# Kernel tuning notes

Hardware: AMD Instinct MI355X
Metric: run time of the kernel (lower is better)

## Reference

```python
import math
import jax, jax.numpy as jnp
import numpy as np

DIM, HEADS, HD = 384, 12, 32
FEAT, WIN, SHIFT = (64, 64), (8, 8), (4, 4)
L = WIN[0] * WIN[1]  # window area = 64
MAX_LOGIT = math.log(1.0 / 0.01)


def _rel_log_coords():
    # pair-wise relative positions, log-spaced (static, numpy)
    coords = np.stack(np.meshgrid(np.arange(WIN[0]), np.arange(WIN[1]), indexing='ij'), 0).reshape(2, -1)
    rel = (coords[:, :, None] - coords[:, None, :]).transpose(1, 2, 0).reshape(-1, 2).astype(np.float32)
    return np.sign(rel) * np.log1p(np.abs(rel))  # [L*L, 2]


def _attn_mask():
    # shifted-window attention mask (static, numpy): 9 regions -> -100 across regions
    H, W = FEAT
    img = np.zeros((H, W), np.int32)
    cnt = 0
    for h0, h1 in ((0, H - WIN[0]), (H - WIN[0], H - SHIFT[0]), (H - SHIFT[0], H)):
        for w0, w1 in ((0, W - WIN[1]), (W - WIN[1], W - SHIFT[1]), (W - SHIFT[1], W)):
            img[h0:h1, w0:w1] = cnt
            cnt += 1
    mw = img.reshape(H // WIN[0], WIN[0], W // WIN[1], WIN[1]).transpose(0, 2, 1, 3).reshape(-1, L)
    diff = mw[:, None, :] - mw[:, :, None]
    return np.where(diff != 0, -100.0, 0.0).astype(np.float32)  # [nW, L, L]


def _ln(x, w, b, eps=1e-5):
    mu = x.mean(-1, keepdims=True)
    var = ((x - mu) ** 2).mean(-1, keepdims=True)
    return (x - mu) / jnp.sqrt(var + eps) * w + b


def setup_inputs() -> dict:
    key = jax.random.key(0)
    ks = jax.random.split(key, 12)
    B = 32
    s = 0.02
    return {
        'x': jax.random.normal(ks[0], (B, FEAT[0], FEAT[1], DIM), jnp.float32),
        'qkv_w': jax.random.normal(ks[1], (3 * DIM, DIM), jnp.float32) * s,
        'qkv_b': jnp.zeros((3 * DIM,), jnp.float32),
        'proj_w': jax.random.normal(ks[2], (DIM, DIM), jnp.float32) * s,
        'proj_b': jnp.zeros((DIM,), jnp.float32),
        'meta_w1': jax.random.normal(ks[3], (384, 2), jnp.float32) * 0.1,
        'meta_b1': jnp.zeros((384,), jnp.float32),
        'meta_w2': jax.random.normal(ks[4], (HEADS, 384), jnp.float32) * 0.1,
        'meta_b2': jnp.zeros((HEADS,), jnp.float32),
        'logit_scale': jnp.full((HEADS,), math.log(10.0), jnp.float32),
        'norm1_w': jnp.ones((DIM,), jnp.float32),
        'norm1_b': jnp.zeros((DIM,), jnp.float32),
        'fc1_w': jax.random.normal(ks[5], (4 * DIM, DIM), jnp.float32) * s,
        'fc1_b': jnp.zeros((4 * DIM,), jnp.float32),
        'fc2_w': jax.random.normal(ks[6], (DIM, 4 * DIM), jnp.float32) * s,
        'fc2_b': jnp.zeros((DIM,), jnp.float32),
        'norm2_w': jnp.ones((DIM,), jnp.float32),
        'norm2_b': jnp.zeros((DIM,), jnp.float32),
    }


def reference(x, qkv_w, qkv_b, proj_w, proj_b, meta_w1, meta_b1, meta_w2, meta_b2,
              logit_scale, norm1_w, norm1_b, fc1_w, fc1_b, fc2_w, fc2_b, norm2_w, norm2_b):
    B, H, W, C = x.shape
    wh, ww = WIN
    # cyclic shift + window partition: (B,H,W,C) -> (B*nW, L, C)
    sx = jnp.roll(x, (-SHIFT[0], -SHIFT[1]), axis=(1, 2))
    xw = sx.reshape(B, H // wh, wh, W // ww, ww, C).transpose(0, 1, 3, 2, 4, 5).reshape(-1, L, C)
    Bw = xw.shape[0]
    qkv = (xw @ qkv_w.T + qkv_b).reshape(Bw, L, 3, HEADS, HD).transpose(2, 0, 3, 1, 4)
    q, k, v = qkv[0], qkv[1], qkv[2]  # [Bw, heads, L, hd]
    # cosine attention
    qn = q / jnp.maximum(jnp.linalg.norm(q, axis=-1, keepdims=True), 1e-12)
    kn = k / jnp.maximum(jnp.linalg.norm(k, axis=-1, keepdims=True), 1e-12)
    attn = jnp.einsum('bhqd,bhkd->bhqk', qn, kn)
    scale = jnp.exp(jnp.minimum(logit_scale, MAX_LOGIT)).reshape(1, HEADS, 1, 1)
    # MLP-based relative position bias
    rel = jnp.asarray(_rel_log_coords())
    bias = jax.nn.relu(rel @ meta_w1.T + meta_b1) @ meta_w2.T + meta_b2  # [L*L, heads]
    bias = bias.T.reshape(HEADS, L, L)
    attn = attn * scale + bias[None]
    # shift mask
    mask = jnp.asarray(_attn_mask())  # [nW, L, L]
    nW = mask.shape[0]
    attn = attn.reshape(Bw // nW, nW, HEADS, L, L) + mask[None, :, None]
    attn = jax.nn.softmax(attn.reshape(Bw, HEADS, L, L), axis=-1)
    out = jnp.einsum('bhqk,bhkd->bhqd', attn, v).transpose(0, 2, 1, 3).reshape(Bw, L, C)
    out = out @ proj_w.T + proj_b
    # window reverse + reverse shift
    out = out.reshape(B, H // wh, W // ww, wh, ww, C).transpose(0, 1, 3, 2, 4, 5).reshape(B, H, W, C)
    out = jnp.roll(out, (SHIFT[0], SHIFT[1]), axis=(1, 2))
    # post-norm residuals (SwinV2Cr style)
    x = x + _ln(out, norm1_w, norm1_b)
    h = jax.nn.gelu(x @ fc1_w.T + fc1_b, approximate=False) @ fc2_w.T + fc2_b
    x = x + _ln(h, norm2_w, norm2_b)
    return x
```

## Files before the change

kernel.cpp:

```cpp
#include <hip/hip_runtime.h>
#include <hip/hip_bf16.h>

typedef __attribute__((ext_vector_type(4))) float f32x4;
typedef __attribute__((ext_vector_type(4))) unsigned int u32x4;
typedef __attribute__((ext_vector_type(8))) __bf16 bf16x8;

#define DEV static __device__ __forceinline__
#define CFENCE() asm volatile("" ::: "memory")

DEV unsigned short f2bf(float f) {
  unsigned u = __builtin_bit_cast(unsigned, f);
  u += 0x7fffu + ((u >> 16) & 1u);
  return (unsigned short)(u >> 16);
}
DEV float bf2f(unsigned short b) {
  return __builtin_bit_cast(float, ((unsigned)b) << 16);
}
DEV unsigned pk2(float a, float b) {
  return (unsigned)f2bf(a) | ((unsigned)f2bf(b) << 16);
}
DEV unsigned cvtpk(float lo, float hi) {
  unsigned r;
  asm("v_cvt_pk_bf16_f32 %0, %1, %2" : "=v"(r) : "v"(lo), "v"(hi));
  return r;
}
DEV float fexp2(float x) {
  float r;
  asm("v_exp_f32 %0, %1" : "=v"(r) : "v"(x));
  return r;
}
DEV float gelu_s(float x) {
  float e = fexp2(-2.45562457f * x);
  return x * __builtin_amdgcn_rcpf(1.f + e);
}
DEV f32x4 mfma16(u32x4 a, u32x4 b, f32x4 c) {
  return __builtin_amdgcn_mfma_f32_16x16x32_bf16(
      __builtin_bit_cast(bf16x8, a), __builtin_bit_cast(bf16x8, b), c, 0, 0, 0);
}
DEV float ssq8(u32x4 c) {
  float s = 0.f;
#pragma unroll
  for (int e = 0; e < 4; e++) {
    float lo = __builtin_bit_cast(float, c[e] << 16);
    float hi = __builtin_bit_cast(float, c[e] & 0xffff0000u);
    s += lo * lo + hi * hi;
  }
  return s;
}
DEV void gload16(const unsigned short* g, unsigned short* l) {
  __builtin_amdgcn_global_load_lds(
      (const __attribute__((address_space(1))) unsigned int*)g,
      (__attribute__((address_space(3))) unsigned int*)l, 16, 0, 0);
}
DEV void waitv(int n) {
  if (n >= 8)
    asm volatile("s_waitcnt vmcnt(8)" ::: "memory");
  else if (n >= 4)
    asm volatile("s_waitcnt vmcnt(4)" ::: "memory");
  else
    asm volatile("s_waitcnt vmcnt(0)" ::: "memory");
}

template <int EPI>
__global__ __launch_bounds__(512, 2) void gemm8(
    const unsigned short* __restrict__ A, const unsigned short* __restrict__ B,
    const float* __restrict__ bias, unsigned short* __restrict__ C,
    int Nc, int K, int nblocks) {
  __shared__ __align__(16) unsigned char smem[131072];
  unsigned short* As0 = (unsigned short*)smem;
  unsigned short* Bs0 = (unsigned short*)(smem + 65536);
  const int bid = blockIdx.x;
  const int mchunk = (gridDim.x >> 3) / nblocks;
  const int xcd = bid & 7, idx = bid >> 3;
  const int nb = idx % nblocks, ml = idx / nblocks;
  const int m0 = (xcd * mchunk + ml) * 256, n0 = nb * 256;
  const int tid = threadIdx.x, w = tid >> 6, l = tid & 63;
  const int lr = l & 15, lg = l >> 4;
  const int wm = (w >> 2) * 128, wn = (w & 3) * 64;
  const int rs = l >> 2;
  const int NT = K >> 5;
  const int gsw = (lg ^ ((lr >> 1) & 3)) * 8;

  auto stA = [&](int b, int kt, int j) {
    int r = j * 128 + w * 16 + rs;
    int sc = ((l & 3) ^ ((r >> 1) & 3)) * 8;
    gload16(A + (size_t)(m0 + r) * K + kt * 32 + sc,
            As0 + b * 8192 + (j * 128 + w * 16) * 32);
  };
  auto stB = [&](int b, int kt, int j) {
    int r = j * 128 + w * 16 + rs;
    int sc = ((l & 3) ^ ((r >> 1) & 3)) * 8;
    gload16(B + (size_t)(n0 + r) * K + kt * 32 + sc,
            Bs0 + b * 8192 + (j * 128 + w * 16) * 32);
  };

  const f32x4 z4 = {0.f, 0.f, 0.f, 0.f};
  f32x4 acc[8][4];
#pragma unroll
  for (int i = 0; i < 8; i++)
#pragma unroll
    for (int j = 0; j < 4; j++) acc[i][j] = z4;
  u32x4 af[8], bf[4];

#pragma unroll
  for (int kp = 0; kp < 3; kp++) {
    stA(kp, kp, 0); stA(kp, kp, 1);
    stB(kp, kp, 0); stB(kp, kp, 1);
  }

  for (int kt = 0; kt < NT; ++kt) {
    const int p = kt & 3;
    waitv(kt + 2 < NT ? 8 : (kt + 1 < NT ? 4 : 0));
    __builtin_amdgcn_s_barrier();
    CFENCE();
    if (kt + 3 < NT) {
      int b3 = (kt + 3) & 3;
      stA(b3, kt + 3, 0); stA(b3, kt + 3, 1);
      stB(b3, kt + 3, 0); stB(b3, kt + 3, 1);
    }
#pragma unroll
    for (int ni = 0; ni < 4; ni++) {
      int R = wn + ni * 16 + lr;
      bf[ni] = *(const u32x4*)&Bs0[p * 8192 + R * 32 + gsw];
    }
#pragma unroll
    for (int mi = 0; mi < 8; mi++) {
      int R = wm + mi * 16 + lr;
      af[mi] = *(const u32x4*)&As0[p * 8192 + R * 32 + gsw];
    }
    __builtin_amdgcn_s_setprio(1);
#pragma unroll
    for (int mi = 0; mi < 8; mi++)
#pragma unroll
      for (int ni = 0; ni < 4; ni++)
        acc[mi][ni] = mfma16(bf[ni], af[mi], acc[mi][ni]);
    __builtin_amdgcn_s_setprio(0);
  }

  __builtin_amdgcn_s_barrier();
  CFENCE();
#pragma unroll
  for (int mh = 0; mh < 2; mh++)
#pragma unroll
    for (int mi = 0; mi < 4; mi++) {
      int mloc = wm + mh * 64 + mi * 16 + lr;
      int msw = mloc & 7;
#pragma unroll
      for (int ni = 0; ni < 4; ni++) {
        f32x4 v = acc[mh * 4 + mi][ni];
        f32x4 bv = *(const f32x4*)&bias[n0 + wn + ni * 16 + lg * 4];
#pragma unroll
        for (int r = 0; r < 4; r++) {
          float t = v[r] + bv[r];
          if (EPI == 1) t = gelu_s(t);
          v[r] = t;
        }
        int nbyte = (wn + ni * 16 + lg * 4) * 2;
        int addr = mloc * 512 + ((((nbyte >> 4) ^ msw) << 4) | (nbyte & 8));
        *(uint2*)(smem + addr) = make_uint2(cvtpk(v[0], v[1]), cvtpk(v[2], v[3]));
      }
    }
  __syncthreads();
#pragma unroll
  for (int c = 0; c < 16; c++) {
    int m = w * 32 + c * 2 + (l >> 5);
    int h = l & 31;
    u32x4 v = *(const u32x4*)(smem + m * 512 + ((h ^ (m & 7)) << 4));
    int n = n0 + h * 8;
    if (n < Nc) *(u32x4*)&C[(size_t)(m0 + m) * Nc + n] = v;
  }
}

template <int MODE>
__global__ __launch_bounds__(512, 2) void gemm_ln8(
    const unsigned short* __restrict__ A, const unsigned short* __restrict__ Bw,
    const float* __restrict__ bias, const float* __restrict__ resf,
    const unsigned short* __restrict__ resb, const float* __restrict__ nw,
    const float* __restrict__ nb, unsigned short* __restrict__ outb,
    float* __restrict__ outf, int K) {
  __shared__ __align__(16) unsigned short As[4][128 * 32];
  __shared__ __align__(16) unsigned short Bs[4][384 * 32];
  const int bid = blockIdx.x;
  const int swz = (bid & 7) * (gridDim.x >> 3) + (bid >> 3);
  const int m0 = swz * 128;
  const int tid = threadIdx.x, w = tid >> 6, l = tid & 63;
  const int lr = l & 15, lg = l >> 4;
  const int wm = (w >> 2) * 64, wn = (w & 3) * 96;
  const int rs = l >> 2;
  const int NT = K >> 5;
  const int gsw = (lg ^ ((lr >> 1) & 3)) * 8;

  auto stA = [&](int b, int kt) {
    int r = w * 16 + rs;
    int sc = ((l & 3) ^ ((r >> 1) & 3)) * 8;
    gload16(A + (size_t)(m0 + r) * K + kt * 32 + sc, &As[b][(w * 16) * 32]);
  };
  auto stB = [&](int b, int kt, int j) {
    int r = j * 128 + w * 16 + rs;
    int sc = ((l & 3) ^ ((r >> 1) & 3)) * 8;
    gload16(Bw + (size_t)r * K + kt * 32 + sc,
            &Bs[b][(j * 128 + w * 16) * 32]);
  };

  const f32x4 z4 = {0.f, 0.f, 0.f, 0.f};
  f32x4 acc[4][6];
#pragma unroll
  for (int i = 0; i < 4; i++)
#pragma unroll
    for (int j = 0; j < 6; j++) acc[i][j] = z4;
  u32x4 af[4], bf[6];

#pragma unroll
  for (int kp = 0; kp < 3; kp++) {
    stA(kp, kp);
    stB(kp, kp, 0); stB(kp, kp, 1); stB(kp, kp, 2);
  }

  for (int kt = 0; kt < NT; ++kt) {
    const int p = kt & 3;
    waitv(kt + 2 < NT ? 8 : (kt + 1 < NT ? 4 : 0));
    __builtin_amdgcn_s_barrier();
    CFENCE();
    if (kt + 3 < NT) {
      int b3 = (kt + 3) & 3;
      stA(b3, kt + 3);
      stB(b3, kt + 3, 0); stB(b3, kt + 3, 1); stB(b3, kt + 3, 2);
    }
#pragma unroll
    for (int nj = 0; nj < 6; nj++) {
      int R = wn + nj * 16 + lr;
      bf[nj] = *(const u32x4*)&Bs[p][R * 32 + gsw];
    }
#pragma unroll
    for (int mi = 0; mi < 4; mi++) {
      int R = wm + mi * 16 + lr;
      af[mi] = *(const u32x4*)&As[p][R * 32 + gsw];
    }
    __builtin_amdgcn_s_setprio(1);
#pragma unroll
    for (int mi = 0; mi < 4; mi++)
#pragma unroll
      for (int nj = 0; nj < 6; nj++)
        acc[mi][nj] = mfma16(af[mi], bf[nj], acc[mi][nj]);
    __builtin_amdgcn_s_setprio(0);
  }

  __syncthreads();
  float bcol[6];
#pragma unroll
  for (int j = 0; j < 6; j++) bcol[j] = bias[wn + j * 16 + lr];
#pragma unroll
  for (int i = 0; i < 4; i++)
#pragma unroll
    for (int j = 0; j < 6; j++)
#pragma unroll
      for (int r = 0; r < 4; r++) acc[i][j][r] += bcol[j];

  float* psum = (float*)(&As[0][0]);
  float* psq  = (float*)(&As[0][1024]);
  const int wn4 = w & 3;
#pragma unroll
  for (int i = 0; i < 4; i++)
#pragma unroll
    for (int r = 0; r < 4; r++) {
      float s1 = 0.f, s2 = 0.f;
#pragma unroll
      for (int j = 0; j < 6; j++) {
        float v = acc[i][j][r];
        s1 += v;
        s2 += v * v;
      }
#pragma unroll
      for (int d = 1; d < 16; d <<= 1) {
        s1 += __shfl_xor(s1, d, 64);
        s2 += __shfl_xor(s2, d, 64);
      }
      if (lr == 0) {
        int row = wm + i * 16 + lg * 4 + r;
        psum[wn4 * 128 + row] = s1;
        psq[wn4 * 128 + row] = s2;
      }
    }
  __syncthreads();

  float wcol[6], b2col[6];
#pragma unroll
  for (int j = 0; j < 6; j++) {
    int col = wn + j * 16 + lr;
    wcol[j] = nw[col];
    b2col[j] = nb[col];
  }
#pragma unroll
  for (int i = 0; i < 4; i++)
#pragma unroll
    for (int r = 0; r < 4; r++) {
      int row = wm + i * 16 + lg * 4 + r;
      float sum = psum[row] + psum[128 + row] + psum[256 + row] + psum[384 + row];
      float sq = psq[row] + psq[128 + row] + psq[256 + row] + psq[384 + row];
      float mu = sum * (1.f / 384.f);
      float rstd = rsqrtf(sq * (1.f / 384.f) - mu * mu + 1e-5f);
      size_t nbase;
      if (MODE == 0) {
        int mrow = m0 + row;
        int bb = mrow >> 12, widx = (mrow >> 6) & 63, tt = mrow & 63;
        int yy = (((widx >> 3) << 3) + (tt >> 3) + 4) & 63;
        int xx = (((widx & 7) << 3) + (tt & 7) + 4) & 63;
        nbase = (size_t)((bb << 12) | (yy << 6) | xx) * 384;
      } else {
        nbase = (size_t)(m0 + row) * 384;
      }
#pragma unroll
      for (int j = 0; j < 6; j++) {
        int col = wn + j * 16 + lr;
        float v = (acc[i][j][r] - mu) * rstd * wcol[j] + b2col[j];
        if (MODE == 0) {
          outb[nbase + col] = f2bf(resf[nbase + col] + v);
        } else {
          outf[nbase + col] = bf2f(resb[nbase + col]) + v;
        }
      }
    }
}

__global__ __launch_bounds__(256) void gather_cvt(
    const float* __restrict__ x, unsigned short* __restrict__ xb) {
  int wv = threadIdx.x >> 6, l = threadIdx.x & 63;
  int m = blockIdx.x * 4 + wv;
  int w = m >> 6, t = m & 63;
  int b = w >> 6, wy = (w >> 3) & 7, wx = w & 7;
  int oy = (wy * 8 + (t >> 3) + 4) & 63;
  int ox = (wx * 8 + (t & 7) + 4) & 63;
  const float2* src =
      (const float2*)(x + (size_t)((((b << 6) | oy) << 6) | ox) * 384 + l * 6);
  float2 f0 = src[0], f1 = src[1], f2 = src[2];
  unsigned* dst = (unsigned*)(xb + (size_t)m * 384 + l * 6);
  dst[0] = pk2(f0.x, f0.y);
  dst[1] = pk2(f1.x, f1.y);
  dst[2] = pk2(f2.x, f2.y);
}

__global__ __launch_bounds__(256, 4) void attn_win(
    const unsigned short* __restrict__ qkv, const float* __restrict__ btab2,
    const float* __restrict__ lscale, unsigned short* __restrict__ aout) {
  __shared__ __align__(16) unsigned short vT[4][32 * 72];
  __shared__ __align__(16) float rnk[4][64];
  const int w = blockIdx.x;
  const int wv = threadIdx.x >> 6, l = threadIdx.x & 63;
  const int h = blockIdx.y * 4 + wv;
  const int lr = l & 15, lg = l >> 4;
  const size_t base = (size_t)w * 64 * 1152 + h * 32;
  const f32x4 z4 = {0.f, 0.f, 0.f, 0.f};

  {
    const u32x4* vp = (const u32x4*)(qkv + base + (size_t)l * 1152 + 768);
#pragma unroll
    for (int c4 = 0; c4 < 4; c4++) {
      u32x4 c = vp[c4];
#pragma unroll
      for (int e = 0; e < 4; e++) {
        vT[wv][(c4 * 8 + e * 2) * 72 + l] = (unsigned short)(c[e] & 0xffffu);
        vT[wv][(c4 * 8 + e * 2 + 1) * 72 + l] = (unsigned short)(c[e] >> 16);
      }
    }
  }
  u32x4 kf[4];
#pragma unroll
  for (int tj = 0; tj < 4; tj++) {
    kf[tj] = *(const u32x4*)(qkv + base + (size_t)(tj * 16 + lr) * 1152 + 384 + lg * 8);
    float s = ssq8(kf[tj]);
    s += __shfl_xor(s, 16, 64);
    s += __shfl_xor(s, 32, 64);
    if (lg == 0) rnk[wv][tj * 16 + lr] = rsqrtf(fmaxf(s, 1e-24f));
  }
  u32x4 qf[4];
  float rnq[4];
#pragma unroll
  for (int ti = 0; ti < 4; ti++) {
    qf[ti] = *(const u32x4*)(qkv + base + (size_t)(ti * 16 + lr) * 1152 + lg * 8);
    float s = ssq8(qf[ti]);
    s += __shfl_xor(s, 16, 64);
    s += __shfl_xor(s, 32, 64);
    rnq[ti] = rsqrtf(fmaxf(s, 1e-24f));
  }
  __syncthreads();

  u32x4 vb[2][2];
#pragma unroll
  for (int kc = 0; kc < 2; kc++)
#pragma unroll
    for (int tj2 = 0; tj2 < 2; tj2++)
      vb[kc][tj2] = *(const u32x4*)(&vT[wv][(tj2 * 16 + lr) * 72 + kc * 32 + lg * 8]);

  const float scl2 = expf(fminf(lscale[h], 4.6051702f)) * 1.44269504f;
  const int wt = ((((w >> 3) & 7) == 7) ? 2 : 0) | (((w & 7) == 7) ? 1 : 0);
  const float* tabh = btab2 + (((size_t)wt * 12 + h) << 12);
  const int s0l = lr + ((l & 16) ? 32 : 0);
  const int s1l = s0l + 16;
  const bool hi = (l & 32) != 0;

#pragma unroll
  for (int ti = 0; ti < 4; ti++) {
    f32x4 sv[4];
#pragma unroll
    for (int tj = 0; tj < 4; tj++) sv[tj] = mfma16(kf[tj], qf[ti], z4);
    const float* tab = tabh + ((ti * 16 + lr) << 6);
    const float cb = rnq[ti] * scl2;
    f32x4 val[4];
    float m = -1e30f;
#pragma unroll
    for (int tj = 0; tj < 4; tj++) {
      f32x4 rk4 = *(const f32x4*)(&rnk[wv][tj * 16 + lg * 4]);
      f32x4 t4 = *(const f32x4*)(tab + tj * 16 + lg * 4);
#pragma unroll
      for (int r = 0; r < 4; r++) {
        float v = sv[tj][r] * (cb * rk4[r]) + t4[r];
        val[tj][r] = v;
        m = fmaxf(m, v);
      }
    }
    m = fmaxf(m, __shfl_xor(m, 16, 64));
    m = fmaxf(m, __shfl_xor(m, 32, 64));
    float den = 0.f;
#pragma unroll
    for (int tj = 0; tj < 4; tj++)
#pragma unroll
      for (int r = 0; r < 4; r++) {
        float p = fexp2(val[tj][r] - m);
        val[tj][r] = p;
        den += p;
      }
    den += __shfl_xor(den, 16, 64);
    den += __shfl_xor(den, 32, 64);
    float rden = 1.f / den;
#pragma unroll
    for (int tj = 0; tj < 4; tj++)
#pragma unroll
      for (int r = 0; r < 4; r++) val[tj][r] *= rden;

    f32x4 o[2] = {z4, z4};
#pragma unroll
    for (int kc = 0; kc < 2; kc++) {
      unsigned yA0 = cvtpk(val[2 * kc][0], val[2 * kc][1]);
      unsigned yA1 = cvtpk(val[2 * kc][2], val[2 * kc][3]);
      unsigned yB0 = cvtpk(val[2 * kc + 1][0], val[2 * kc + 1][1]);
      unsigned yB1 = cvtpk(val[2 * kc + 1][2], val[2 * kc + 1][3]);
      unsigned a0 = __shfl((int)yA0, s0l, 64), b0 = __shfl((int)yB0, s0l, 64);
      unsigned a1 = __shfl((int)yA1, s0l, 64), b1 = __shfl((int)yB1, s0l, 64);
      unsigned a2 = __shfl((int)yA0, s1l, 64), b2 = __shfl((int)yB0, s1l, 64);
      unsigned a3 = __shfl((int)yA1, s1l, 64), b3 = __shfl((int)yB1, s1l, 64);
      u32x4 pa = {hi ? b0 : a0, hi ? b1 : a1, hi ? b2 : a2, hi ? b3 : a3};
#pragma unroll
      for (int tj2 = 0; tj2 < 2; tj2++) o[tj2] = mfma16(pa, vb[kc][tj2], o[tj2]);
    }
#pragma unroll
    for (int tj2 = 0; tj2 < 2; tj2++)
#pragma unroll
      for (int r = 0; r < 4; r++)
        aout[(size_t)(w * 64 + ti * 16 + lg * 4 + r) * 384 + h * 32 + tj2 * 16 + lr] =
            f2bf(o[tj2][r]);
  }
}

__global__ __launch_bounds__(256) void btab2_kernel(
    const float* __restrict__ w1, const float* __restrict__ b1,
    const float* __restrict__ w2, const float* __restrict__ b2,
    float* __restrict__ btab2) {
  int p = blockIdx.x * 256 + threadIdx.x;
  int i = p >> 6, j = p & 63;
  float dy = (float)((i >> 3) - (j >> 3));
  float dx = (float)((i & 7) - (j & 7));
  float r0 = (dy > 0.f ? 1.f : (dy < 0.f ? -1.f : 0.f)) * log1pf(fabsf(dy));
  float r1 = (dx > 0.f ? 1.f : (dx < 0.f ? -1.f : 0.f)) * log1pf(fabsf(dx));
  float acc[12];
#pragma unroll
  for (int hh = 0; hh < 12; hh++) acc[hh] = b2[hh];
  for (int c = 0; c < 384; c++) {
    float hv = w1[c * 2] * r0 + w1[c * 2 + 1] * r1 + b1[c];
    hv = fmaxf(hv, 0.f);
#pragma unroll
    for (int hh = 0; hh < 12; hh++) acc[hh] += hv * w2[hh * 384 + c];
  }
  bool ddy = ((i >> 3) >= 4) != ((j >> 3) >= 4);
  bool ddx = ((i & 7) >= 4) != ((j & 7) >= 4);
  const float L2E = 1.44269504f;
#pragma unroll
  for (int wt = 0; wt < 4; wt++) {
    float mask = ((((wt >> 1) != 0) && ddy) || (((wt & 1) != 0) && ddx)) ? -100.f : 0.f;
#pragma unroll
    for (int hh = 0; hh < 12; hh++)
      btab2[(((size_t)wt * 12 + hh) << 12) + p] = (acc[hh] + mask) * L2E;
  }
}

__global__ __launch_bounds__(256) void prep_kernel(
    const float* __restrict__ qkv_w, const float* __restrict__ proj_w,
    const float* __restrict__ w1, const float* __restrict__ w2,
    const float* __restrict__ qkv_b, unsigned short* __restrict__ wqb,
    unsigned short* __restrict__ wpb, unsigned short* __restrict__ w1b,
    unsigned short* __restrict__ w2b, float* __restrict__ qbp) {
  int i = blockIdx.x * 256 + threadIdx.x;
  if (i < 491520) {
    wqb[i] = (i < 442368) ? f2bf(qkv_w[i]) : (unsigned short)0;
  } else if (i < 638976) {
    int j = i - 491520;
    wpb[j] = f2bf(proj_w[j]);
  } else if (i < 1228800) {
    int j = i - 638976;
    w1b[j] = f2bf(w1[j]);
  } else if (i < 1818624) {
    int j = i - 1228800;
    w2b[j] = f2bf(w2[j]);
  } else if (i < 1819904) {
    int j = i - 1818624;
    qbp[j] = (j < 1152) ? qkv_b[j] : 0.f;
  }
}

extern "C" void kernel_launch(void* const* d_in, const int* in_sizes, int n_in,
                              void* d_out, int out_size, void* d_ws,
                              size_t ws_size, hipStream_t stream) {
  (void)in_sizes; (void)n_in; (void)out_size; (void)ws_size;
  const float* x      = (const float*)d_in[0];
  const float* qkv_w  = (const float*)d_in[1];
  const float* qkv_b  = (const float*)d_in[2];
  const float* proj_w = (const float*)d_in[3];
  const float* proj_b = (const float*)d_in[4];
  const float* mw1    = (const float*)d_in[5];
  const float* mb1    = (const float*)d_in[6];
  const float* mw2    = (const float*)d_in[7];
  const float* mb2    = (const float*)d_in[8];
  const float* lsc    = (const float*)d_in[9];
  const float* n1w    = (const float*)d_in[10];
  const float* n1b    = (const float*)d_in[11];
  const float* w1     = (const float*)d_in[12];
  const float* b1     = (const float*)d_in[13];
  const float* w2     = (const float*)d_in[14];
  const float* b2     = (const float*)d_in[15];
  const float* n2w    = (const float*)d_in[16];
  const float* n2b    = (const float*)d_in[17];

  char* ws = (char*)d_ws;
  unsigned short* wqb  = (unsigned short*)(ws + 0);
  unsigned short* wpb  = (unsigned short*)(ws + 1048576);
  unsigned short* w1b  = (unsigned short*)(ws + 1441792);
  unsigned short* w2b  = (unsigned short*)(ws + 2621440);
  float* qbp           = (float*)(ws + 3801088);
  float* btab2         = (float*)(ws + 3866624);
  unsigned short* xb   = (unsigned short*)(ws + 4718592);
  unsigned short* qkvb = (unsigned short*)(ws + 105381888);
  unsigned short* att  = (unsigned short*)(ws + 440926208);
  unsigned short* y1b  = xb;
  unsigned short* hb   = qkvb;
  float* yout = (float*)d_out;

  prep_kernel<<<dim3(7109), 256, 0, stream>>>(qkv_w, proj_w, w1, w2, qkv_b,
                                              wqb, wpb, w1b, w2b, qbp);
  btab2_kernel<<<dim3(16), 256, 0, stream>>>(mw1, mb1, mw2, mb2, btab2);
  gather_cvt<<<dim3(32768), 256, 0, stream>>>(x, xb);

  gemm8<0><<<dim3(2560), 512, 0, stream>>>(xb, wqb, qbp, qkvb, 1152, 384, 5);
  attn_win<<<dim3(2048, 3), 256, 0, stream>>>(qkvb, btab2, lsc, att);
  gemm_ln8<0><<<dim3(1024), 512, 0, stream>>>(
      att, wpb, proj_b, x, nullptr, n1w, n1b, y1b, nullptr, 384);
  gemm8<1><<<dim3(3072), 512, 0, stream>>>(y1b, w1b, b1, hb, 1536, 384, 6);
  gemm_ln8<1><<<dim3(1024), 512, 0, stream>>>(
      hb, w2b, b2, nullptr, y1b, n2w, n2b, nullptr, yout, 1536);
}
```

Baseline: 1.166 ms.

## Switch GEMMs to double-buffered LDS staging and merge prep kernels into one launch

Both GEMM kernels move from a 4-stage, 3-ahead global-to-LDS prefetch ring to a 2-stage double buffer with a full vmcnt(0) wait each iteration. This halves shared memory per block, and the gemm8 epilogue is split into two halves so it still fits in the smaller LDS. The three preprocessing kernels (gather/convert, weight conversion, bias table) are merged into one launch to cut launch overhead. The shallower pipeline exposes more global-load latency, traded against lower LDS use and possibly higher occupancy.

```diff
diff --git a/kernel.cpp b/kernel.cpp
--- a/kernel.cpp
+++ b/kernel.cpp
@@ -51,14 +51,6 @@
   __builtin_amdgcn_global_load_lds(
       (const __attribute__((address_space(1))) unsigned int*)g,
       (__attribute__((address_space(3))) unsigned int*)l, 16, 0, 0);
-}
-DEV void waitv(int n) {
-  if (n >= 8)
-    asm volatile("s_waitcnt vmcnt(8)" ::: "memory");
-  else if (n >= 4)
-    asm volatile("s_waitcnt vmcnt(4)" ::: "memory");
-  else
-    asm volatile("s_waitcnt vmcnt(0)" ::: "memory");
 }
 
 template <int EPI>
@@ -66,9 +58,9 @@
     const unsigned short* __restrict__ A, const unsigned short* __restrict__ B,
     const float* __restrict__ bias, unsigned short* __restrict__ C,
     int Nc, int K, int nblocks) {
-  __shared__ __align__(16) unsigned char smem[131072];
+  __shared__ __align__(16) unsigned char smem[65536];
   unsigned short* As0 = (unsigned short*)smem;
-  unsigned short* Bs0 = (unsigned short*)(smem + 65536);
+  unsigned short* Bs0 = (unsigned short*)(smem + 32768);
   const int bid = blockIdx.x;
   const int mchunk = (gridDim.x >> 3) / nblocks;
   const int xcd = bid & 7, idx = bid >> 3;
@@ -78,20 +70,19 @@
   const int lr = l & 15, lg = l >> 4;
   const int wm = (w >> 2) * 128, wn = (w & 3) * 64;
   const int rs = l >> 2;
+  const int gs = ((l & 3) ^ ((l >> 3) & 3)) * 8;
+  const int gsw = (lg ^ ((lr >> 1) & 3)) * 8;
   const int NT = K >> 5;
-  const int gsw = (lg ^ ((lr >> 1) & 3)) * 8;
-
-  auto stA = [&](int b, int kt, int j) {
-    int r = j * 128 + w * 16 + rs;
-    int sc = ((l & 3) ^ ((r >> 1) & 3)) * 8;
-    gload16(A + (size_t)(m0 + r) * K + kt * 32 + sc,
-            As0 + b * 8192 + (j * 128 + w * 16) * 32);
-  };
-  auto stB = [&](int b, int kt, int j) {
-    int r = j * 128 + w * 16 + rs;
-    int sc = ((l & 3) ^ ((r >> 1) & 3)) * 8;
-    gload16(B + (size_t)(n0 + r) * K + kt * 32 + sc,
-            Bs0 + b * 8192 + (j * 128 + w * 16) * 32);
+
+  auto stage = [&](int p, int kt) {
+#pragma unroll
+    for (int j = 0; j < 2; j++) {
+      int rb = j * 128 + w * 16;
+      gload16(A + (size_t)(m0 + rb + rs) * K + kt * 32 + gs,
+              As0 + p * 8192 + rb * 32);
+      gload16(B + (size_t)(n0 + rb + rs) * K + kt * 32 + gs,
+              Bs0 + p * 8192 + rb * 32);
+    }
   };
 
   const f32x4 z4 = {0.f, 0.f, 0.f, 0.f};
@@ -102,32 +93,19 @@
     for (int j = 0; j < 4; j++) acc[i][j] = z4;
   u32x4 af[8], bf[4];
 
-#pragma unroll
-  for (int kp = 0; kp < 3; kp++) {
-    stA(kp, kp, 0); stA(kp, kp, 1);
-    stB(kp, kp, 0); stB(kp, kp, 1);
-  }
-
+  stage(0, 0);
   for (int kt = 0; kt < NT; ++kt) {
-    const int p = kt & 3;
-    waitv(kt + 2 < NT ? 8 : (kt + 1 < NT ? 4 : 0));
+    const int p = kt & 1;
+    asm volatile("s_waitcnt vmcnt(0)" ::: "memory");
     __builtin_amdgcn_s_barrier();
     CFENCE();
-    if (kt + 3 < NT) {
-      int b3 = (kt + 3) & 3;
-      stA(b3, kt + 3, 0); stA(b3, kt + 3, 1);
-      stB(b3, kt + 3, 0); stB(b3, kt + 3, 1);
-    }
-#pragma unroll
-    for (int ni = 0; ni < 4; ni++) {
-      int R = wn + ni * 16 + lr;
-      bf[ni] = *(const u32x4*)&Bs0[p * 8192 + R * 32 + gsw];
-    }
-#pragma unroll
-    for (int mi = 0; mi < 8; mi++) {
-      int R = wm + mi * 16 + lr;
-      af[mi] = *(const u32x4*)&As0[p * 8192 + R * 32 + gsw];
-    }
+    if (kt + 1 < NT) stage(p ^ 1, kt + 1);
+#pragma unroll
+    for (int ni = 0; ni < 4; ni++)
+      bf[ni] = *(const u32x4*)&Bs0[p * 8192 + (wn + ni * 16 + lr) * 32 + gsw];
+#pragma unroll
+    for (int mi = 0; mi < 8; mi++)
+      af[mi] = *(const u32x4*)&As0[p * 8192 + (wm + mi * 16 + lr) * 32 + gsw];
     __builtin_amdgcn_s_setprio(1);
 #pragma unroll
     for (int mi = 0; mi < 8; mi++)
@@ -135,39 +113,45 @@
       for (int ni = 0; ni < 4; ni++)
         acc[mi][ni] = mfma16(bf[ni], af[mi], acc[mi][ni]);
     __builtin_amdgcn_s_setprio(0);
-  }
-
-  __builtin_amdgcn_s_barrier();
-  CFENCE();
-#pragma unroll
-  for (int mh = 0; mh < 2; mh++)
-#pragma unroll
-    for (int mi = 0; mi < 4; mi++) {
-      int mloc = wm + mh * 64 + mi * 16 + lr;
-      int msw = mloc & 7;
-#pragma unroll
-      for (int ni = 0; ni < 4; ni++) {
-        f32x4 v = acc[mh * 4 + mi][ni];
-        f32x4 bv = *(const f32x4*)&bias[n0 + wn + ni * 16 + lg * 4];
-#pragma unroll
-        for (int r = 0; r < 4; r++) {
-          float t = v[r] + bv[r];
-          if (EPI == 1) t = gelu_s(t);
-          v[r] = t;
+    asm volatile("s_waitcnt lgkmcnt(0)" ::: "memory");
+    CFENCE();
+  }
+
+#pragma unroll
+  for (int half = 0; half < 2; half++) {
+    __syncthreads();
+    if ((w >> 2) == half) {
+#pragma unroll
+      for (int mi = 0; mi < 8; mi++) {
+        int rl = mi * 16 + lr;
+        int msw = rl & 7;
+#pragma unroll
+        for (int ni = 0; ni < 4; ni++) {
+          f32x4 v = acc[mi][ni];
+          f32x4 bv = *(const f32x4*)&bias[n0 + wn + ni * 16 + lg * 4];
+#pragma unroll
+          for (int r = 0; r < 4; r++) {
+            float t = v[r] + bv[r];
+            if (EPI == 1) t = gelu_s(t);
+            v[r] = t;
+          }
+          int nbyte = (wn + ni * 16 + lg * 4) * 2;
+          int addr = rl * 512 + ((((nbyte >> 4) ^ msw) << 4) | (nbyte & 8));
+          *(uint2*)(smem + addr) =
+              make_uint2(cvtpk(v[0], v[1]), cvtpk(v[2], v[3]));
         }
-        int nbyte = (wn + ni * 16 + lg * 4) * 2;
-        int addr = mloc * 512 + ((((nbyte >> 4) ^ msw) << 4) | (nbyte & 8));
-        *(uint2*)(smem + addr) = make_uint2(cvtpk(v[0], v[1]), cvtpk(v[2], v[3]));
-      }
-    }
-  __syncthreads();
-#pragma unroll
-  for (int c = 0; c < 16; c++) {
-    int m = w * 32 + c * 2 + (l >> 5);
-    int h = l & 31;
-    u32x4 v = *(const u32x4*)(smem + m * 512 + ((h ^ (m & 7)) << 4));
-    int n = n0 + h * 8;
-    if (n < Nc) *(u32x4*)&C[(size_t)(m0 + m) * Nc + n] = v;
+      }
+    }
+    __syncthreads();
+#pragma unroll
+    for (int c = 0; c < 8; c++) {
+      int mloc = w * 16 + c * 2 + (l >> 5);
+      int h = l & 31;
+      u32x4 v = *(const u32x4*)(smem + mloc * 512 + ((h ^ (mloc & 7)) << 4));
+      int n = n0 + h * 8;
+      if (n < Nc)
+        *(u32x4*)&C[(size_t)(m0 + half * 128 + mloc) * Nc + n] = v;
+    }
   }
 }
 
@@ -178,8 +162,8 @@
     const unsigned short* __restrict__ resb, const float* __restrict__ nw,
     const float* __restrict__ nb, unsigned short* __restrict__ outb,
     float* __restrict__ outf, int K) {
-  __shared__ __align__(16) unsigned short As[4][128 * 32];
-  __shared__ __align__(16) unsigned short Bs[4][384 * 32];
+  __shared__ __align__(16) unsigned short As[2][128 * 32];
+  __shared__ __align__(16) unsigned short Bs[2][384 * 32];
   const int bid = blockIdx.x;
   const int swz = (bid & 7) * (gridDim.x >> 3) + (bid >> 3);
   const int m0 = swz * 128;
@@ -187,19 +171,18 @@
   const int lr = l & 15, lg = l >> 4;
   const int wm = (w >> 2) * 64, wn = (w & 3) * 96;
   const int rs = l >> 2;
+  const int gs = ((l & 3) ^ ((l >> 3) & 3)) * 8;
+  const int gsw = (lg ^ ((lr >> 1) & 3)) * 8;
   const int NT = K >> 5;
-  const int gsw = (lg ^ ((lr >> 1) & 3)) * 8;
-
-  auto stA = [&](int b, int kt) {
-    int r = w * 16 + rs;
-    int sc = ((l & 3) ^ ((r >> 1) & 3)) * 8;
-    gload16(A + (size_t)(m0 + r) * K + kt * 32 + sc, &As[b][(w * 16) * 32]);
-  };
-  auto stB = [&](int b, int kt, int j) {
-    int r = j * 128 + w * 16 + rs;
-    int sc = ((l & 3) ^ ((r >> 1) & 3)) * 8;
-    gload16(Bw + (size_t)r * K + kt * 32 + sc,
-            &Bs[b][(j * 128 + w * 16) * 32]);
+
+  auto stage = [&](int p, int kt) {
+    gload16(A + (size_t)(m0 + w * 16 + rs) * K + kt * 32 + gs,
+            &As[p][(w * 16) * 32]);
+#pragma unroll
+    for (int j = 0; j < 3; j++) {
+      int rb = j * 128 + w * 16;
+      gload16(Bw + (size_t)(rb + rs) * K + kt * 32 + gs, &Bs[p][rb * 32]);
+    }
   };
 
   const f32x4 z4 = {0.f, 0.f, 0.f, 0.f};
@@ -210,32 +193,19 @@
     for (int j = 0; j < 6; j++) acc[i][j] = z4;
   u32x4 af[4], bf[6];
 
-#pragma unroll
-  for (int kp = 0; kp < 3; kp++) {
-    stA(kp, kp);
-    stB(kp, kp, 0); stB(kp, kp, 1); stB(kp, kp, 2);
-  }
-
+  stage(0, 0);
   for (int kt = 0; kt < NT; ++kt) {
-    const int p = kt & 3;
-    waitv(kt + 2 < NT ? 8 : (kt + 1 < NT ? 4 : 0));
+    const int p = kt & 1;
+    asm volatile("s_waitcnt vmcnt(0)" ::: "memory");
     __builtin_amdgcn_s_barrier();
     CFENCE();
-    if (kt + 3 < NT) {
-      int b3 = (kt + 3) & 3;
-      stA(b3, kt + 3);
-      stB(b3, kt + 3, 0); stB(b3, kt + 3, 1); stB(b3, kt + 3, 2);
-    }
-#pragma unroll
-    for (int nj = 0; nj < 6; nj++) {
-      int R = wn + nj * 16 + lr;
-      bf[nj] = *(const u32x4*)&Bs[p][R * 32 + gsw];
-    }
-#pragma unroll
-    for (int mi = 0; mi < 4; mi++) {
-      int R = wm + mi * 16 + lr;
-      af[mi] = *(const u32x4*)&As[p][R * 32 + gsw];
-    }
+    if (kt + 1 < NT) stage(p ^ 1, kt + 1);
+#pragma unroll
+    for (int nj = 0; nj < 6; nj++)
+      bf[nj] = *(const u32x4*)&Bs[p][(wn + nj * 16 + lr) * 32 + gsw];
+#pragma unroll
+    for (int mi = 0; mi < 4; mi++)
+      af[mi] = *(const u32x4*)&As[p][(wm + mi * 16 + lr) * 32 + gsw];
     __builtin_amdgcn_s_setprio(1);
 #pragma unroll
     for (int mi = 0; mi < 4; mi++)
@@ -243,6 +213,8 @@
       for (int nj = 0; nj < 6; nj++)
         acc[mi][nj] = mfma16(af[mi], bf[nj], acc[mi][nj]);
     __builtin_amdgcn_s_setprio(0);
+    asm volatile("s_waitcnt lgkmcnt(0)" ::: "memory");
+    CFENCE();
   }
 
   __syncthreads();
@@ -322,23 +294,6 @@
     }
 }
 
-__global__ __launch_bounds__(256) void gather_cvt(
-    const float* __restrict__ x, unsigned short* __restrict__ xb) {
-  int wv = threadIdx.x >> 6, l = threadIdx.x & 63;
-  int m = blockIdx.x * 4 + wv;
-  int w = m >> 6, t = m & 63;
-  int b = w >> 6, wy = (w >> 3) & 7, wx = w & 7;
-  int oy = (wy * 8 + (t >> 3) + 4) & 63;
-  int ox = (wx * 8 + (t & 7) + 4) & 63;
-  const float2* src =
-      (const float2*)(x + (size_t)((((b << 6) | oy) << 6) | ox) * 384 + l * 6);
-  float2 f0 = src[0], f1 = src[1], f2 = src[2];
-  unsigned* dst = (unsigned*)(xb + (size_t)m * 384 + l * 6);
-  dst[0] = pk2(f0.x, f0.y);
-  dst[1] = pk2(f1.x, f1.y);
-  dst[2] = pk2(f2.x, f2.y);
-}
-
 __global__ __launch_bounds__(256, 4) void attn_win(
     const unsigned short* __restrict__ qkv, const float* __restrict__ btab2,
     const float* __restrict__ lscale, unsigned short* __restrict__ aout) {
@@ -461,58 +416,74 @@
   }
 }
 
-__global__ __launch_bounds__(256) void btab2_kernel(
-    const float* __restrict__ w1, const float* __restrict__ b1,
-    const float* __restrict__ w2, const float* __restrict__ b2,
-    float* __restrict__ btab2) {
-  int p = blockIdx.x * 256 + threadIdx.x;
-  int i = p >> 6, j = p & 63;
-  float dy = (float)((i >> 3) - (j >> 3));
-  float dx = (float)((i & 7) - (j & 7));
-  float r0 = (dy > 0.f ? 1.f : (dy < 0.f ? -1.f : 0.f)) * log1pf(fabsf(dy));
-  float r1 = (dx > 0.f ? 1.f : (dx < 0.f ? -1.f : 0.f)) * log1pf(fabsf(dx));
-  float acc[12];
-#pragma unroll
-  for (int hh = 0; hh < 12; hh++) acc[hh] = b2[hh];
-  for (int c = 0; c < 384; c++) {
-    float hv = w1[c * 2] * r0 + w1[c * 2 + 1] * r1 + b1[c];
-    hv = fmaxf(hv, 0.f);
-#pragma unroll
-    for (int hh = 0; hh < 12; hh++) acc[hh] += hv * w2[hh * 384 + c];
-  }
-  bool ddy = ((i >> 3) >= 4) != ((j >> 3) >= 4);
-  bool ddx = ((i & 7) >= 4) != ((j & 7) >= 4);
-  const float L2E = 1.44269504f;
-#pragma unroll
-  for (int wt = 0; wt < 4; wt++) {
-    float mask = ((((wt >> 1) != 0) && ddy) || (((wt & 1) != 0) && ddx)) ? -100.f : 0.f;
-#pragma unroll
-    for (int hh = 0; hh < 12; hh++)
-      btab2[(((size_t)wt * 12 + hh) << 12) + p] = (acc[hh] + mask) * L2E;
-  }
-}
-
-__global__ __launch_bounds__(256) void prep_kernel(
+__global__ __launch_bounds__(256) void prepass_kernel(
+    const float* __restrict__ x, unsigned short* __restrict__ xb,
     const float* __restrict__ qkv_w, const float* __restrict__ proj_w,
     const float* __restrict__ w1, const float* __restrict__ w2,
     const float* __restrict__ qkv_b, unsigned short* __restrict__ wqb,
     unsigned short* __restrict__ wpb, unsigned short* __restrict__ w1b,
-    unsigned short* __restrict__ w2b, float* __restrict__ qbp) {
-  int i = blockIdx.x * 256 + threadIdx.x;
-  if (i < 491520) {
-    wqb[i] = (i < 442368) ? f2bf(qkv_w[i]) : (unsigned short)0;
-  } else if (i < 638976) {
-    int j = i - 491520;
-    wpb[j] = f2bf(proj_w[j]);
-  } else if (i < 1228800) {
-    int j = i - 638976;
-    w1b[j] = f2bf(w1[j]);
-  } else if (i < 1818624) {
-    int j = i - 1228800;
-    w2b[j] = f2bf(w2[j]);
-  } else if (i < 1819904) {
-    int j = i - 1818624;
-    qbp[j] = (j < 1152) ? qkv_b[j] : 0.f;
+    unsigned short* __restrict__ w2b, float* __restrict__ qbp,
+    const float* __restrict__ mw1, const float* __restrict__ mb1,
+    const float* __restrict__ mw2, const float* __restrict__ mb2,
+    float* __restrict__ btab2) {
+  const int blk = blockIdx.x;
+  if (blk < 32768) {
+    int wv = threadIdx.x >> 6, l = threadIdx.x & 63;
+    int m = blk * 4 + wv;
+    int w = m >> 6, t = m & 63;
+    int b = w >> 6, wy = (w >> 3) & 7, wx = w & 7;
+    int oy = (wy * 8 + (t >> 3) + 4) & 63;
+    int ox = (wx * 8 + (t & 7) + 4) & 63;
+    const float2* src =
+        (const float2*)(x + (size_t)((((b << 6) | oy) << 6) | ox) * 384 + l * 6);
+    float2 f0 = src[0], f1 = src[1], f2 = src[2];
+    unsigned* dst = (unsigned*)(xb + (size_t)m * 384 + l * 6);
+    dst[0] = pk2(f0.x, f0.y);
+    dst[1] = pk2(f1.x, f1.y);
+    dst[2] = pk2(f2.x, f2.y);
+  } else if (blk < 39877) {
+    int i = (blk - 32768) * 256 + threadIdx.x;
+    if (i < 491520) {
+      wqb[i] = (i < 442368) ? f2bf(qkv_w[i]) : (unsigned short)0;
+    } else if (i < 638976) {
+      int j = i - 491520;
+      wpb[j] = f2bf(proj_w[j]);
+    } else if (i < 1228800) {
+      int j = i - 638976;
+      w1b[j] = f2bf(w1[j]);
+    } else if (i < 1818624) {
+      int j = i - 1228800;
+      w2b[j] = f2bf(w2[j]);
+    } else if (i < 1819904) {
+      int j = i - 1818624;
+      qbp[j] = (j < 1152) ? qkv_b[j] : 0.f;
+    }
+  } else {
+    int p = (blk - 39877) * 256 + threadIdx.x;
+    int i = p >> 6, j = p & 63;
+    float dy = (float)((i >> 3) - (j >> 3));
+    float dx = (float)((i & 7) - (j & 7));
+    float r0 = (dy > 0.f ? 1.f : (dy < 0.f ? -1.f : 0.f)) * log1pf(fabsf(dy));
+    float r1 = (dx > 0.f ? 1.f : (dx < 0.f ? -1.f : 0.f)) * log1pf(fabsf(dx));
+    float acc[12];
+#pragma unroll
+    for (int hh = 0; hh < 12; hh++) acc[hh] = mb2[hh];
+    for (int c = 0; c < 384; c++) {
+      float hv = mw1[c * 2] * r0 + mw1[c * 2 + 1] * r1 + mb1[c];
+      hv = fmaxf(hv, 0.f);
+#pragma unroll
+      for (int hh = 0; hh < 12; hh++) acc[hh] += hv * mw2[hh * 384 + c];
+    }
+    bool ddy = ((i >> 3) >= 4) != ((j >> 3) >= 4);
+    bool ddx = ((i & 7) >= 4) != ((j & 7) >= 4);
+    const float L2E = 1.44269504f;
+#pragma unroll
+    for (int wt = 0; wt < 4; wt++) {
+      float mask = ((((wt >> 1) != 0) && ddy) || (((wt & 1) != 0) && ddx)) ? -100.f : 0.f;
+#pragma unroll
+      for (int hh = 0; hh < 12; hh++)
+        btab2[(((size_t)wt * 12 + hh) << 12) + p] = (acc[hh] + mask) * L2E;
+    }
   }
 }
 
@@ -553,10 +524,9 @@
   unsigned short* hb   = qkvb;
   float* yout = (float*)d_out;
 
-  prep_kernel<<<dim3(7109), 256, 0, stream>>>(qkv_w, proj_w, w1, w2, qkv_b,
-                                              wqb, wpb, w1b, w2b, qbp);
-  btab2_kernel<<<dim3(16), 256, 0, stream>>>(mw1, mb1, mw2, mb2, btab2);
-  gather_cvt<<<dim3(32768), 256, 0, stream>>>(x, xb);
+  prepass_kernel<<<dim3(39893), 256, 0, stream>>>(
+      x, xb, qkv_w, proj_w, w1, w2, qkv_b, wqb, wpb, w1b, w2b, qbp,
+      mw1, mb1, mw2, mb2, btab2);
 
   gemm8<0><<<dim3(2560), 512, 0, stream>>>(xb, wqb, qbp, qkvb, 1152, 384, 5);
   attn_win<<<dim3(2048, 3), 256, 0, stream>>>(qkvb, btab2, lsc, att);
```

Measured after the change: 1.225 ms. 5.1% more time.
